# Performance work log

Hardware: AMD Instinct MI355X
Metric: run time of the kernel (lower is better)

Reference implementation:

```python
import jax, jax.numpy as jnp
import numpy as np

NEG_SLOPE = 0.125


def _ssm_step(u, s, A, Bm, C, D):
    # u: [N,2]; s: [N,2,4,2] (re/im); A,Bm: [2,4,2]; C: [1,2,4,2]; D: [1,2]
    sr, si = s[..., 0], s[..., 1]
    Ar, Ai = A[..., 0], A[..., 1]
    Br, Bi = Bm[..., 0], Bm[..., 1]
    uf = u[..., None]  # [N,2,1]
    # next_state = A * state + B * u  (complex elementwise)
    nr = Ar * sr - Ai * si + Br * uf
    ni = Ar * si + Ai * sr + Bi * uf
    Cr, Ci = C[..., 0], C[..., 1]  # [c=1, h=2, f=4]
    # y = 2 * Re( sum_f C[c,h,f] * next_state[n,h,f] ) -> [N, c, h]
    yr = jnp.einsum('chf,nhf->nch', Cr, nr) - jnp.einsum('chf,nhf->nch', Ci, ni)
    y = 2.0 * yr + u[:, None, :] * D  # [N,1,2]
    y = y.reshape(u.shape[0], 2)  # (c h) flatten with c=1
    ns = jnp.stack([nr, ni], axis=-1)  # [N,2,4,2]
    return y, ns


def _act(x):
    return jnp.where(x >= 0, x, NEG_SLOPE * x)


def setup_inputs() -> dict:
    key = jax.random.key(0)
    ks = jax.random.split(key, 9)
    B = 1048576
    return {
        'x': jax.random.normal(ks[0], (B, 4), dtype=jnp.float32),
        'states': jax.random.normal(ks[1], (4, B, 2, 4, 2), dtype=jnp.float32),
        'fc1_w': jax.random.normal(ks[2], (2, 4), dtype=jnp.float32),
        'fc1_b': jax.random.normal(ks[3], (2,), dtype=jnp.float32),
        'fc_w': jax.random.normal(ks[4], (5, 2, 2), dtype=jnp.float32),
        'fc_b': jax.random.normal(ks[5], (5, 2), dtype=jnp.float32),
        'A': jax.random.normal(ks[6], (4, 2, 4, 2), dtype=jnp.float32),
        'Bm': jax.random.normal(ks[7], (4, 2, 4, 2), dtype=jnp.float32),
        'C': jax.random.normal(ks[8], (4, 1, 2, 4, 2), dtype=jnp.float32),
        'D': jax.random.normal(jax.random.fold_in(key, 99), (4, 1, 2), dtype=jnp.float32),
    }


def reference(x, states, fc1_w, fc1_b, fc_w, fc_b, A, Bm, C, D):
    # fc1 (input layer): [N,4] -> [N,2]
    h = x @ fc1_w.T + fc1_b
    new_states = []
    for i in range(4):
        h, ns = _ssm_step(h, states[i], A[i], Bm[i], C[i], D[i])
        new_states.append(ns)
        h = _act(h)
        h = h @ fc_w[i].T + fc_b[i]
    # fc10
    h = h @ fc_w[4].T + fc_b[4]
    return h, jnp.stack(new_states, axis=0)
```

## Files before the change

### kernel.cpp

```cpp
#include <hip/hip_runtime.h>


constexpr float NEG_SLOPE = 0.125f;

typedef float fv4 __attribute__((ext_vector_type(4)));

__global__ __launch_bounds__(256) void ssm_fused(
    const float* __restrict__ x,
    const float* __restrict__ states,
    const float* __restrict__ fc1_w,
    const float* __restrict__ fc1_b,
    const float* __restrict__ fc_w,
    const float* __restrict__ fc_b,
    const float* __restrict__ A,
    const float* __restrict__ Bm,
    const float* __restrict__ Cm,
    const float* __restrict__ Dm,
    float* __restrict__ out_h,
    float* __restrict__ out_states,
    int B)
{
    __shared__ __align__(16) float w[240];
    const int t = threadIdx.x;
    if (t < 240) {
        float v;
        if (t < 8)        v = fc1_w[t];
        else if (t < 10)  v = fc1_b[t - 8];
        else if (t < 30)  v = fc_w[t - 10];
        else if (t < 40)  v = fc_b[t - 30];
        else if (t < 104) v = A[t - 40];
        else if (t < 168) v = Bm[t - 104];
        else if (t < 232) v = Cm[t - 168];
        else              v = Dm[t - 232];
        w[t] = v;
    }
    __syncthreads();

    const int g = blockIdx.x * 256 + t;
    const int n = g >> 2;
    const int c = g & 3;
    if (n >= B) return;

    const float4 xv = ((const float4*)x)[n];
    float h0 = w[8] + xv.x * w[0] + xv.y * w[1] + xv.z * w[2] + xv.w * w[3];
    float h1 = w[9] + xv.x * w[4] + xv.y * w[5] + xv.z * w[6] + xv.w * w[7];

    const float* wA  = w + 40;
    const float* wB  = w + 104;
    const float* wC  = w + 168;
    const float* wD  = w + 232;
    const float* wfc = w + 10;
    const float* wfb = w + 30;
    const bool hi = (c & 2) != 0;

#pragma unroll
    for (int i = 0; i < 4; ++i) {
        const size_t base = ((size_t)i * (size_t)B + (size_t)n) * 16 + (size_t)(c * 4);
        const fv4 s  = __builtin_nontemporal_load((const fv4*)(states + base));
        const fv4 a  = *(const fv4*)(wA + i * 16 + c * 4);
        const fv4 b  = *(const fv4*)(wB + i * 16 + c * 4);
        const fv4 cc = *(const fv4*)(wC + i * 16 + c * 4);

        const float u = hi ? h1 : h0;
        const float nr0 = a.x * s.x - a.y * s.y + b.x * u;
        const float ni0 = a.x * s.y + a.y * s.x + b.y * u;
        const float nr1 = a.z * s.z - a.w * s.w + b.z * u;
        const float ni1 = a.z * s.w + a.w * s.z + b.w * u;

        float part = cc.x * nr0 - cc.y * ni0 + cc.z * nr1 - cc.w * ni1;
        part += __shfl_xor(part, 1);
        const float other = __shfl_xor(part, 2);
        const float acc0 = hi ? other : part;
        const float acc1 = hi ? part  : other;

        float y0 = 2.f * acc0 + h0 * wD[i * 2 + 0];
        float y1 = 2.f * acc1 + h1 * wD[i * 2 + 1];
        y0 = (y0 >= 0.f) ? y0 : NEG_SLOPE * y0;
        y1 = (y1 >= 0.f) ? y1 : NEG_SLOPE * y1;
        const float nh0 = wfb[i * 2 + 0] + wfc[i * 4 + 0] * y0 + wfc[i * 4 + 1] * y1;
        const float nh1 = wfb[i * 2 + 1] + wfc[i * 4 + 2] * y0 + wfc[i * 4 + 3] * y1;
        h0 = nh0; h1 = nh1;

        fv4 nsv; nsv.x = nr0; nsv.y = ni0; nsv.z = nr1; nsv.w = ni1;
        __builtin_nontemporal_store(nsv, (fv4*)(out_states + base));
    }

    if (c == 0) {
        const float o0 = wfb[8] + wfc[16] * h0 + wfc[17] * h1;
        const float o1 = wfb[9] + wfc[18] * h0 + wfc[19] * h1;
        ((float2*)out_h)[n] = make_float2(o0, o1);
    }
}

extern "C" void kernel_launch(void* const* d_in, const int* in_sizes, int n_in,
                              void* d_out, int out_size, void* d_ws, size_t ws_size,
                              hipStream_t stream) {
    const float* x      = (const float*)d_in[0];
    const float* states = (const float*)d_in[1];
    const float* fc1_w  = (const float*)d_in[2];
    const float* fc1_b  = (const float*)d_in[3];
    const float* fc_w   = (const float*)d_in[4];
    const float* fc_b   = (const float*)d_in[5];
    const float* A      = (const float*)d_in[6];
    const float* Bm     = (const float*)d_in[7];
    const float* Cm     = (const float*)d_in[8];
    const float* Dm     = (const float*)d_in[9];
    const int B = in_sizes[0] / 4;

    float* out_h      = (float*)d_out;
    float* out_states = (float*)d_out + (size_t)2 * (size_t)B;

    const long long threads = 4LL * (long long)B;
    dim3 grid((unsigned)((threads + 255) / 256)), block(256);
    hipLaunchKernelGGL(ssm_fused, grid, block, 0, stream,
                       x, states, fc1_w, fc1_b, fc_w, fc_b, A, Bm, Cm, Dm,
                       out_h, out_states, B);
}
```

Baseline: 465.1 us.

## Process two rows per thread with all state loads issued upfront and DPP quad shuffles

```diff
diff --git a/kernel.cpp b/kernel.cpp
--- a/kernel.cpp
+++ b/kernel.cpp
@@ -4,6 +4,11 @@
 constexpr float NEG_SLOPE = 0.125f;
 
 typedef float fv4 __attribute__((ext_vector_type(4)));
+
+template<int CTRL>
+__device__ __forceinline__ float qperm(float v) {
+    return __int_as_float(__builtin_amdgcn_mov_dpp(__float_as_int(v), CTRL, 0xF, 0xF, true));
+}
 
 __global__ __launch_bounds__(256) void ssm_fused(
     const float* __restrict__ x,
@@ -37,13 +42,36 @@
     __syncthreads();
 
     const int g = blockIdx.x * 256 + t;
-    const int n = g >> 2;
+    const int q = g >> 2;
     const int c = g & 3;
-    if (n >= B) return;
+    const int r0cnt = (B + 1) >> 1;
+    if (q >= r0cnt) return;
 
-    const float4 xv = ((const float4*)x)[n];
-    float h0 = w[8] + xv.x * w[0] + xv.y * w[1] + xv.z * w[2] + xv.w * w[3];
-    float h1 = w[9] + xv.x * w[4] + xv.y * w[5] + xv.z * w[6] + xv.w * w[7];
+    const int n0 = q;
+    const int n1 = q + r0cnt;
+    const bool has1 = (n1 < B);
+
+    const int B16 = B * 16;
+    const int c4  = c * 4;
+    const int f0  = n0 * 16 + c4;
+    const int f1  = n1 * 16 + c4;
+
+    fv4 s0[4], s1[4];
+#pragma unroll
+    for (int i = 0; i < 4; ++i) {
+        s0[i] = *(const fv4*)(states + f0 + i * B16);
+        if (has1) s1[i] = *(const fv4*)(states + f1 + i * B16);
+    }
+
+    const float4 xv0 = ((const float4*)x)[n0];
+    float hA0 = w[8] + xv0.x * w[0] + xv0.y * w[1] + xv0.z * w[2] + xv0.w * w[3];
+    float hA1 = w[9] + xv0.x * w[4] + xv0.y * w[5] + xv0.z * w[6] + xv0.w * w[7];
+    float hB0 = 0.f, hB1 = 0.f;
+    if (has1) {
+        const float4 xv1 = ((const float4*)x)[n1];
+        hB0 = w[8] + xv1.x * w[0] + xv1.y * w[1] + xv1.z * w[2] + xv1.w * w[3];
+        hB1 = w[9] + xv1.x * w[4] + xv1.y * w[5] + xv1.z * w[6] + xv1.w * w[7];
+    }
 
     const float* wA  = w + 40;
     const float* wB  = w + 104;
@@ -55,40 +83,65 @@
 
 #pragma unroll
     for (int i = 0; i < 4; ++i) {
-        const size_t base = ((size_t)i * (size_t)B + (size_t)n) * 16 + (size_t)(c * 4);
-        const fv4 s  = __builtin_nontemporal_load((const fv4*)(states + base));
-        const fv4 a  = *(const fv4*)(wA + i * 16 + c * 4);
-        const fv4 b  = *(const fv4*)(wB + i * 16 + c * 4);
-        const fv4 cc = *(const fv4*)(wC + i * 16 + c * 4);
+        const fv4 a  = *(const fv4*)(wA + i * 16 + c4);
+        const fv4 b  = *(const fv4*)(wB + i * 16 + c4);
+        const fv4 cw = *(const fv4*)(wC + i * 16 + c4);
+        const float d0  = wD[i * 2 + 0], d1  = wD[i * 2 + 1];
+        const float w00 = wfc[i * 4 + 0], w01 = wfc[i * 4 + 1];
+        const float w10 = wfc[i * 4 + 2], w11 = wfc[i * 4 + 3];
+        const float fb0 = wfb[i * 2 + 0], fb1 = wfb[i * 2 + 1];
 
-        const float u = hi ? h1 : h0;
-        const float nr0 = a.x * s.x - a.y * s.y + b.x * u;
-        const float ni0 = a.x * s.y + a.y * s.x + b.y * u;
-        const float nr1 = a.z * s.z - a.w * s.w + b.z * u;
-        const float ni1 = a.z * s.w + a.w * s.z + b.w * u;
-
-        float part = cc.x * nr0 - cc.y * ni0 + cc.z * nr1 - cc.w * ni1;
-        part += __shfl_xor(part, 1);
-        const float other = __shfl_xor(part, 2);
-        const float acc0 = hi ? other : part;
-        const float acc1 = hi ? part  : other;
-
-        float y0 = 2.f * acc0 + h0 * wD[i * 2 + 0];
-        float y1 = 2.f * acc1 + h1 * wD[i * 2 + 1];
-        y0 = (y0 >= 0.f) ? y0 : NEG_SLOPE * y0;
-        y1 = (y1 >= 0.f) ? y1 : NEG_SLOPE * y1;
-        const float nh0 = wfb[i * 2 + 0] + wfc[i * 4 + 0] * y0 + wfc[i * 4 + 1] * y1;
-        const float nh1 = wfb[i * 2 + 1] + wfc[i * 4 + 2] * y0 + wfc[i * 4 + 3] * y1;
-        h0 = nh0; h1 = nh1;
-
-        fv4 nsv; nsv.x = nr0; nsv.y = ni0; nsv.z = nr1; nsv.w = ni1;
-        __builtin_nontemporal_store(nsv, (fv4*)(out_states + base));
+        {
+            const fv4 s = s0[i];
+            const float u = hi ? hA1 : hA0;
+            const float nr0 = a.x * s.x - a.y * s.y + b.x * u;
+            const float ni0 = a.x * s.y + a.y * s.x + b.y * u;
+            const float nr1 = a.z * s.z - a.w * s.w + b.z * u;
+            const float ni1 = a.z * s.w + a.w * s.z + b.w * u;
+            float part = cw.x * nr0 - cw.y * ni0 + cw.z * nr1 - cw.w * ni1;
+            part += qperm<0xB1>(part);
+            const float other = qperm<0x4E>(part);
+            const float acc0 = hi ? other : part;
+            const float acc1 = hi ? part  : other;
+            float y0 = 2.f * acc0 + hA0 * d0;
+            float y1 = 2.f * acc1 + hA1 * d1;
+            y0 = (y0 >= 0.f) ? y0 : NEG_SLOPE * y0;
+            y1 = (y1 >= 0.f) ? y1 : NEG_SLOPE * y1;
+            hA0 = fb0 + w00 * y0 + w01 * y1;
+            hA1 = fb1 + w10 * y0 + w11 * y1;
+            fv4 nsv; nsv.x = nr0; nsv.y = ni0; nsv.z = nr1; nsv.w = ni1;
+            __builtin_nontemporal_store(nsv, (fv4*)(out_states + f0 + i * B16));
+        }
+        if (has1) {
+            const fv4 s = s1[i];
+            const float u = hi ? hB1 : hB0;
+            const float nr0 = a.x * s.x - a.y * s.y + b.x * u;
+            const float ni0 = a.x * s.y + a.y * s.x + b.y * u;
+            const float nr1 = a.z * s.z - a.w * s.w + b.z * u;
+            const float ni1 = a.z * s.w + a.w * s.z + b.w * u;
+            float part = cw.x * nr0 - cw.y * ni0 + cw.z * nr1 - cw.w * ni1;
+            part += qperm<0xB1>(part);
+            const float other = qperm<0x4E>(part);
+            const float acc0 = hi ? other : part;
+            const float acc1 = hi ? part  : other;
+            float y0 = 2.f * acc0 + hB0 * d0;
+            float y1 = 2.f * acc1 + hB1 * d1;
+            y0 = (y0 >= 0.f) ? y0 : NEG_SLOPE * y0;
+            y1 = (y1 >= 0.f) ? y1 : NEG_SLOPE * y1;
+            hB0 = fb0 + w00 * y0 + w01 * y1;
+            hB1 = fb1 + w10 * y0 + w11 * y1;
+            fv4 nsv; nsv.x = nr0; nsv.y = ni0; nsv.z = nr1; nsv.w = ni1;
+            __builtin_nontemporal_store(nsv, (fv4*)(out_states + f1 + i * B16));
+        }
     }
 
     if (c == 0) {
-        const float o0 = wfb[8] + wfc[16] * h0 + wfc[17] * h1;
-        const float o1 = wfb[9] + wfc[18] * h0 + wfc[19] * h1;
-        ((float2*)out_h)[n] = make_float2(o0, o1);
+        float2* o2 = (float2*)out_h;
+        o2[n0] = make_float2(wfb[8] + wfc[16] * hA0 + wfc[17] * hA1,
+                             wfb[9] + wfc[18] * hA0 + wfc[19] * hA1);
+        if (has1)
+            o2[n1] = make_float2(wfb[8] + wfc[16] * hB0 + wfc[17] * hB1,
+                                 wfb[9] + wfc[18] * hB0 + wfc[19] * hB1);
     }
 }
 
@@ -110,7 +163,8 @@
     float* out_h      = (float*)d_out;
     float* out_states = (float*)d_out + (size_t)2 * (size_t)B;
 
-    const long long threads = 4LL * (long long)B;
+    const long long r0cnt = ((long long)B + 1) / 2;
+    const long long threads = 4LL * r0cnt;
     dim3 grid((unsigned)((threads + 255) / 256)), block(256);
     hipLaunchKernelGGL(ssm_fused, grid, block, 0, stream,
                        x, states, fc1_w, fc1_b, fc_w, fc_b, A, Bm, Cm, Dm,
```

After: 504.4 us. +8.4%, slower.
